# Performance work log

Measured on AMD Instinct MI355X. Metric: run time of the kernel, lower is better.

## Reference

```python
import jax, jax.numpy as jnp
import numpy as np

IN_F = 2048
OUT_F = 2048
BATCH = 16384
BASE_SPARSITY = 0.02
REVIVAL_DENSITY = 0.2   # rows for dead ('low') output neurons
RELIEF_DENSITY = 0.15   # cols for saturated ('high') input neurons
DEAD = np.arange(16)                      # 'low' extrema (row indices)
SATURATED = np.arange(100, 900, 100)      # 'high' extrema (col indices)


def _make_mask(key):
    k1, k2, k3 = jax.random.split(key, 3)
    base = (jax.random.uniform(k1, (OUT_F, IN_F)) < BASE_SPARSITY).astype(jnp.float32)
    patch = jnp.zeros((OUT_F, IN_F), jnp.float32)
    # dense-ish rows for dead output neurons
    row_patch = (jax.random.uniform(k2, (len(DEAD), IN_F)) < REVIVAL_DENSITY).astype(jnp.float32)
    patch = patch.at[jnp.asarray(DEAD), :].set(row_patch)
    # dense-ish cols for saturated input neurons (overwrite, matching torch order)
    col_patch = (jax.random.uniform(k3, (OUT_F, len(SATURATED))) < RELIEF_DENSITY).astype(jnp.float32)
    patch = patch.at[:, jnp.asarray(SATURATED)].set(col_patch)
    return jnp.maximum(base, patch)


def setup_inputs() -> dict:
    key = jax.random.key(0)
    kx, kw, km = jax.random.split(key, 3)
    x = jax.random.normal(kx, (BATCH, IN_F), dtype=jnp.float32)
    # kaiming_uniform_(a=sqrt(5)) -> U(-bound, bound), bound = sqrt(6/((1+a^2)*fan_in)) = 1/sqrt(fan_in)
    bound = 1.0 / np.sqrt(IN_F)
    weight = jax.random.uniform(kw, (OUT_F, IN_F), minval=-bound, maxval=bound, dtype=jnp.float32)
    bias = jnp.zeros((OUT_F,), jnp.float32)
    mask = _make_mask(km)
    return {"x": x, "weight": weight, "bias": bias, "mask": mask}


def reference(x, weight, bias, mask):
    # F.linear(x, weight * mask, bias): y = x @ (W*M)^T + b
    return jnp.einsum('bi,oi->bo', x, weight * mask) + bias
```

## Files before the change

### kernel.cpp

```cpp
#include <hip/hip_runtime.h>
#include <stdint.h>

#define BATCH 16384
#define IN_F 2048
#define OUT_F 2048

typedef unsigned short u16;
typedef __attribute__((ext_vector_type(8))) short bf16x8;
typedef __attribute__((ext_vector_type(4))) float f32x4;

__device__ __forceinline__ u16 f2bf(float f) {
  union { float f; uint32_t u; } v; v.f = f;
  uint32_t u = v.u;
  u += 0x7FFFu + ((u >> 16) & 1u);
  return (u16)(u >> 16);
}


__global__ void cvt_fused(const float4* __restrict__ x, const float4* __restrict__ w,
                          const float4* __restrict__ m, u16* __restrict__ xb,
                          u16* __restrict__ wb) {
  const int NX = BATCH * IN_F / 4;
  int i = blockIdx.x * 256 + threadIdx.x;
  if (i < NX) {
    float4 v = x[i];
    uint2 p;
    p.x = (uint32_t)f2bf(v.x) | ((uint32_t)f2bf(v.y) << 16);
    p.y = (uint32_t)f2bf(v.z) | ((uint32_t)f2bf(v.w) << 16);
    ((uint2*)xb)[i] = p;
  } else {
    int j = i - NX;
    float4 wv = w[j];
    float4 mv = m[j];
    uint2 p;
    p.x = (uint32_t)f2bf(wv.x * mv.x) | ((uint32_t)f2bf(wv.y * mv.y) << 16);
    p.y = (uint32_t)f2bf(wv.z * mv.z) | ((uint32_t)f2bf(wv.w * mv.w) << 16);
    ((uint2*)wb)[j] = p;
  }
}


__device__ __forceinline__ void async_cp16(const void* g, void* l) {
  __builtin_amdgcn_global_load_lds(
      (const __attribute__((address_space(1))) void*)g,
      (__attribute__((address_space(3))) void*)l,
      16, 0, 0);
}


#define BK 32
#define NT (IN_F / BK)

__global__ __launch_bounds__(512, 2) void gemm_bf16(const u16* __restrict__ A,
                                                    const u16* __restrict__ B,
                                                    const float* __restrict__ bias,
                                                    float* __restrict__ C) {
  __shared__ __align__(128) char smem[4 * 32768];
  const int K = IN_F, N = OUT_F;
  const int tid = threadIdx.x;
  const int lane = tid & 63, wave = tid >> 6;
  const int wm = wave >> 2;
  const int wn = wave & 3;
  const long bn = (long)blockIdx.x * 256;
  const long bm = (long)blockIdx.y * 256;

  const int sr = tid >> 2, sc = tid & 3;
  const int scs = sc ^ ((sr >> 1) & 3);
  const u16* gA = A + (bm + sr) * K + scs * 8;
  const u16* gB = B + (bn + sr) * K + scs * 8;
  const long hiK = 128L * K;
  const int ldst = tid * 16;

  auto stageA = [&](int slot, int kt) {
    char* sb = smem + slot * 32768;
    const long ko = (long)kt * BK;
    async_cp16(gA + ko, sb + ldst);
    async_cp16(gA + hiK + ko, sb + 8192 + ldst);
  };
  auto stageB = [&](int slot, int kt) {
    char* sb = smem + slot * 32768 + 16384;
    const long ko = (long)kt * BK;
    async_cp16(gB + ko, sb + ldst);
    async_cp16(gB + hiK + ko, sb + 8192 + ldst);
  };

  const int rl = lane & 15;
  const int q = lane >> 4;
  const int fb = rl * 64 + ((q ^ ((rl >> 1) & 3)) * 16);
  const int aoff = wm * 8192;
  const int boff = 16384 + wn * 4096;

  f32x4 acc[8][4];
#pragma unroll
  for (int i = 0; i < 8; i++)
#pragma unroll
    for (int j = 0; j < 4; j++)
#pragma unroll
      for (int r = 0; r < 4; r++) acc[i][j][r] = 0.0f;

  stageA(0, 0); stageB(0, 0);
  stageA(1, 1); stageB(1, 1);
  stageA(2, 2); stageB(2, 2);
  asm volatile("s_waitcnt vmcnt(4)" ::: "memory");
  __builtin_amdgcn_s_barrier();

  bf16x8 afA[4], bfA[4], afB[4], bfB[4];
#pragma unroll
  for (int i = 0; i < 4; i++) afA[i] = *(const bf16x8*)(smem + aoff + i * 1024 + fb);
#pragma unroll
  for (int j = 0; j < 4; j++) bfA[j] = *(const bf16x8*)(smem + boff + j * 1024 + fb);

#define BODY(T, curA, curB, nxtA, nxtB)                                          \
  do {                                                                           \
    const int t_ = (T);                                                          \
    const int slot_ = t_ & 3, s1_ = (t_ + 1) & 3, s3_ = (t_ + 3) & 3;            \
    const int kt3_ = (t_ + 3 < NT) ? t_ + 3 : NT - 1;                            \
    const char* sA_ = smem + slot_ * 32768 + aoff;                               \
    const char* sA1_ = smem + s1_ * 32768 + aoff;                                \
    const char* sB1_ = smem + s1_ * 32768 + boff;                                \
    stageA(s3_, kt3_);                                                           \
    stageB(s3_, kt3_);                                                           \
    bf16x8 af1_[4];                                                              \
    _Pragma("unroll")                                                            \
    for (int i = 0; i < 4; i++) af1_[i] = *(const bf16x8*)(sA_ + 4096 + i * 1024 + fb); \
    __builtin_amdgcn_s_setprio(1);                                               \
    _Pragma("unroll")                                                            \
    for (int i = 0; i < 4; i++)                                                  \
      _Pragma("unroll")                                                          \
      for (int j = 0; j < 4; j++)                                                \
        acc[i][j] = __builtin_amdgcn_mfma_f32_16x16x32_bf16(curA[i], curB[j], acc[i][j], 0, 0, 0); \
    __builtin_amdgcn_s_setprio(0);                                               \
    _Pragma("unroll")                                                            \
    for (int i = 0; i < 4; i++) nxtA[i] = *(const bf16x8*)(sA1_ + i * 1024 + fb); \
    _Pragma("unroll")                                                            \
    for (int j = 0; j < 4; j++) nxtB[j] = *(const bf16x8*)(sB1_ + j * 1024 + fb); \
    __builtin_amdgcn_s_setprio(1);                                               \
    _Pragma("unroll")                                                            \
    for (int i = 0; i < 4; i++)                                                  \
      _Pragma("unroll")                                                          \
      for (int j = 0; j < 4; j++)                                                \
        acc[4 + i][j] = __builtin_amdgcn_mfma_f32_16x16x32_bf16(af1_[i], curB[j], acc[4 + i][j], 0, 0, 0); \
    __builtin_amdgcn_s_setprio(0);                                               \
    asm volatile("s_waitcnt vmcnt(4)" ::: "memory");                             \
    __builtin_amdgcn_s_barrier();                                                \
  } while (0)

  for (int t = 0; t < NT; t += 2) {
    BODY(t, afA, bfA, afB, bfB);
    BODY(t + 1, afB, bfB, afA, bfA);
  }
#undef BODY

  asm volatile("s_waitcnt vmcnt(0)" ::: "memory");

  const int cn = lane & 15;
  const int crow = (lane >> 4) * 4;
#pragma unroll
  for (int j = 0; j < 4; j++) {
    const long n = bn + wn * 64 + j * 16 + cn;
    const float bv = bias[n];
#pragma unroll
    for (int i = 0; i < 8; i++) {
      const long m0 = bm + wm * 128 + i * 16 + crow;
      float* cp = C + m0 * N + n;
#pragma unroll
      for (int r = 0; r < 4; r++)
        cp[(long)r * N] = acc[i][j][r] + bv;
    }
  }
}


__global__ void naive_kernel(const float* __restrict__ x, const float* __restrict__ w,
                             const float* __restrict__ bias, const float* __restrict__ m,
                             float* __restrict__ out) {
  size_t idx = (size_t)blockIdx.x * 256 + threadIdx.x;
  int o = (int)(idx % OUT_F);
  size_t b = idx / OUT_F;
  float s = bias[o];
  const float* xr = x + b * IN_F;
  const float* wr = w + (size_t)o * IN_F;
  const float* mr = m + (size_t)o * IN_F;
  for (int k = 0; k < IN_F; k++) s += xr[k] * wr[k] * mr[k];
  out[idx] = s;
}

extern "C" void kernel_launch(void* const* d_in, const int* in_sizes, int n_in,
                              void* d_out, int out_size, void* d_ws, size_t ws_size,
                              hipStream_t stream) {
  const float* x = (const float*)d_in[0];
  const float* w = (const float*)d_in[1];
  const float* bias = (const float*)d_in[2];
  const float* mask = (const float*)d_in[3];
  float* out = (float*)d_out;

  const size_t xb_elems = (size_t)BATCH * IN_F;
  const size_t wm_elems = (size_t)OUT_F * IN_F;
  const size_t need = (xb_elems + wm_elems) * sizeof(u16);

  if (ws_size >= need) {
    u16* xb = (u16*)d_ws;
    u16* wm = xb + xb_elems;
    const uint32_t nblk = (uint32_t)((xb_elems + wm_elems) / 4 / 256);
    cvt_fused<<<nblk, 256, 0, stream>>>((const float4*)x, (const float4*)w,
                                        (const float4*)mask, xb, wm);
    gemm_bf16<<<dim3(OUT_F / 256, BATCH / 256), 512, 0, stream>>>(xb, wm, bias, out);
  } else {
    naive_kernel<<<(uint32_t)(((size_t)BATCH * OUT_F) / 256), 256, 0, stream>>>(x, w, bias, mask, out);
  }
}
```

Before: 360.6 us.

## Switch GEMM inner loop from 16x16x32 to 32x32x16 bf16 MFMA tiles

Replaces the 16x16x32 MFMA fragments with 32x32x16 bf16 MFMA, which changes the per-wave fragment layout, the LDS read addressing (with the same swizzle), the accumulator shape and the output store mapping. The loop is also unrolled by four so that LDS slot indices become compile-time constants. The larger MFMA is meant to cut the number of instructions and the LDS fragment reads per FLOP, but the epilogue now issues strided stores in a different pattern.

```diff
diff --git a/kernel.cpp b/kernel.cpp
--- a/kernel.cpp
+++ b/kernel.cpp
@@ -7,7 +7,7 @@
 
 typedef unsigned short u16;
 typedef __attribute__((ext_vector_type(8))) short bf16x8;
-typedef __attribute__((ext_vector_type(4))) float f32x4;
+typedef __attribute__((ext_vector_type(16))) float f32x16;
 
 __device__ __forceinline__ u16 f2bf(float f) {
   union { float f; uint32_t u; } v; v.f = f;
@@ -84,19 +84,26 @@
     async_cp16(gB + hiK + ko, sb + 8192 + ldst);
   };
 
-  const int rl = lane & 15;
-  const int q = lane >> 4;
-  const int fb = rl * 64 + ((q ^ ((rl >> 1) & 3)) * 16);
-  const int aoff = wm * 8192;
-  const int boff = 16384 + wn * 4096;
-
-  f32x4 acc[8][4];
-#pragma unroll
-  for (int i = 0; i < 8; i++)
-#pragma unroll
-    for (int j = 0; j < 4; j++)
-#pragma unroll
-      for (int r = 0; r < 4; r++) acc[i][j][r] = 0.0f;
+  const int r32 = lane & 31;
+  const int kq = lane >> 5;
+  const int xr = (r32 >> 1) & 3;
+  const int co0 = ((0 + kq) ^ xr) * 16;
+  const int co1 = ((2 + kq) ^ xr) * 16;
+  const int abase = wm * 8192 + r32 * 64;
+  const int bbase = 16384 + wn * 4096 + r32 * 64;
+
+#define LDA(SLOT, SUB, KS) \
+  (*(const bf16x8*)(smem + (SLOT) * 32768 + abase + (SUB) * 2048 + ((KS) ? co1 : co0)))
+#define LDB(SLOT, J, KS) \
+  (*(const bf16x8*)(smem + (SLOT) * 32768 + bbase + (J) * 2048 + ((KS) ? co1 : co0)))
+
+  f32x16 acc[4][2];
+#pragma unroll
+  for (int i = 0; i < 4; i++)
+#pragma unroll
+    for (int j = 0; j < 2; j++)
+#pragma unroll
+      for (int r = 0; r < 16; r++) acc[i][j][r] = 0.0f;
 
   stageA(0, 0); stageB(0, 0);
   stageA(1, 1); stageB(1, 1);
@@ -106,66 +113,82 @@
 
   bf16x8 afA[4], bfA[4], afB[4], bfB[4];
 #pragma unroll
-  for (int i = 0; i < 4; i++) afA[i] = *(const bf16x8*)(smem + aoff + i * 1024 + fb);
-#pragma unroll
-  for (int j = 0; j < 4; j++) bfA[j] = *(const bf16x8*)(smem + boff + j * 1024 + fb);
-
-#define BODY(T, curA, curB, nxtA, nxtB)                                          \
+  for (int i = 0; i < 2; i++) {
+    afA[i * 2 + 0] = LDA(0, i, 0);
+    afA[i * 2 + 1] = LDA(0, i, 1);
+    bfA[i * 2 + 0] = LDB(0, i, 0);
+    bfA[i * 2 + 1] = LDB(0, i, 1);
+  }
+
+#define BODY(T, SLOT, curA, curB, nxtA, nxtB)                                    \
   do {                                                                           \
     const int t_ = (T);                                                          \
-    const int slot_ = t_ & 3, s1_ = (t_ + 1) & 3, s3_ = (t_ + 3) & 3;            \
-    const int kt3_ = (t_ + 3 < NT) ? t_ + 3 : NT - 1;                            \
-    const char* sA_ = smem + slot_ * 32768 + aoff;                               \
-    const char* sA1_ = smem + s1_ * 32768 + aoff;                                \
-    const char* sB1_ = smem + s1_ * 32768 + boff;                                \
-    stageA(s3_, kt3_);                                                           \
-    stageB(s3_, kt3_);                                                           \
+    const int kt3_ = (t_ + 3 < NT) ? (t_ + 3) : (NT - 1);                        \
+    stageA(((SLOT) + 3) & 3, kt3_);                                              \
+    stageB(((SLOT) + 3) & 3, kt3_);                                              \
     bf16x8 af1_[4];                                                              \
     _Pragma("unroll")                                                            \
-    for (int i = 0; i < 4; i++) af1_[i] = *(const bf16x8*)(sA_ + 4096 + i * 1024 + fb); \
+    for (int i = 0; i < 2; i++) {                                                \
+      af1_[i * 2 + 0] = LDA(SLOT, 2 + i, 0);                                     \
+      af1_[i * 2 + 1] = LDA(SLOT, 2 + i, 1);                                     \
+    }                                                                            \
     __builtin_amdgcn_s_setprio(1);                                               \
     _Pragma("unroll")                                                            \
-    for (int i = 0; i < 4; i++)                                                  \
+    for (int ks = 0; ks < 2; ks++)                                               \
       _Pragma("unroll")                                                          \
-      for (int j = 0; j < 4; j++)                                                \
-        acc[i][j] = __builtin_amdgcn_mfma_f32_16x16x32_bf16(curA[i], curB[j], acc[i][j], 0, 0, 0); \
+      for (int i = 0; i < 2; i++)                                                \
+        _Pragma("unroll")                                                        \
+        for (int j = 0; j < 2; j++)                                              \
+          acc[i][j] = __builtin_amdgcn_mfma_f32_32x32x16_bf16(                   \
+              curA[i * 2 + ks], curB[j * 2 + ks], acc[i][j], 0, 0, 0);           \
     __builtin_amdgcn_s_setprio(0);                                               \
     _Pragma("unroll")                                                            \
-    for (int i = 0; i < 4; i++) nxtA[i] = *(const bf16x8*)(sA1_ + i * 1024 + fb); \
-    _Pragma("unroll")                                                            \
-    for (int j = 0; j < 4; j++) nxtB[j] = *(const bf16x8*)(sB1_ + j * 1024 + fb); \
+    for (int i = 0; i < 2; i++) {                                                \
+      nxtA[i * 2 + 0] = LDA(((SLOT) + 1) & 3, i, 0);                             \
+      nxtA[i * 2 + 1] = LDA(((SLOT) + 1) & 3, i, 1);                             \
+      nxtB[i * 2 + 0] = LDB(((SLOT) + 1) & 3, i, 0);                             \
+      nxtB[i * 2 + 1] = LDB(((SLOT) + 1) & 3, i, 1);                             \
+    }                                                                            \
     __builtin_amdgcn_s_setprio(1);                                               \
     _Pragma("unroll")                                                            \
-    for (int i = 0; i < 4; i++)                                                  \
+    for (int ks = 0; ks < 2; ks++)                                               \
       _Pragma("unroll")                                                          \
-      for (int j = 0; j < 4; j++)                                                \
-        acc[4 + i][j] = __builtin_amdgcn_mfma_f32_16x16x32_bf16(af1_[i], curB[j], acc[4 + i][j], 0, 0, 0); \
+      for (int i = 0; i < 2; i++)                                                \
+        _Pragma("unroll")                                                        \
+        for (int j = 0; j < 2; j++)                                              \
+          acc[2 + i][j] = __builtin_amdgcn_mfma_f32_32x32x16_bf16(               \
+              af1_[i * 2 + ks], curB[j * 2 + ks], acc[2 + i][j], 0, 0, 0);       \
     __builtin_amdgcn_s_setprio(0);                                               \
     asm volatile("s_waitcnt vmcnt(4)" ::: "memory");                             \
     __builtin_amdgcn_s_barrier();                                                \
   } while (0)
 
-  for (int t = 0; t < NT; t += 2) {
-    BODY(t, afA, bfA, afB, bfB);
-    BODY(t + 1, afB, bfB, afA, bfA);
+  for (int t = 0; t < NT; t += 4) {
+    BODY(t + 0, 0, afA, bfA, afB, bfB);
+    BODY(t + 1, 1, afB, bfB, afA, bfA);
+    BODY(t + 2, 2, afA, bfA, afB, bfB);
+    BODY(t + 3, 3, afB, bfB, afA, bfA);
   }
 #undef BODY
+#undef LDA
+#undef LDB
 
   asm volatile("s_waitcnt vmcnt(0)" ::: "memory");
 
-  const int cn = lane & 15;
-  const int crow = (lane >> 4) * 4;
-#pragma unroll
-  for (int j = 0; j < 4; j++) {
-    const long n = bn + wn * 64 + j * 16 + cn;
+  const int c32 = lane & 31;
+  const int rq4 = (lane >> 5) * 4;
+#pragma unroll
+  for (int j = 0; j < 2; j++) {
+    const long n = bn + wn * 64 + j * 32 + c32;
     const float bv = bias[n];
 #pragma unroll
-    for (int i = 0; i < 8; i++) {
-      const long m0 = bm + wm * 128 + i * 16 + crow;
-      float* cp = C + m0 * N + n;
-#pragma unroll
-      for (int r = 0; r < 4; r++)
-        cp[(long)r * N] = acc[i][j][r] + bv;
+    for (int i = 0; i < 4; i++) {
+      const long m0 = bm + wm * 128 + i * 32 + rq4;
+#pragma unroll
+      for (int reg = 0; reg < 16; reg++) {
+        const int row = (reg & 3) + 8 * (reg >> 2);
+        C[(m0 + row) * (long)N + n] = acc[i][j][reg] + bv;
+      }
     }
   }
 }
```

After: 365.8 us. No clear change (+1.4%).

## Load B fragments directly from global into registers, keep only A in LDS

Applied to the files above, without the earlier changes.

The weight (B) operand no longer goes through shared memory. Each wave loads its B fragments straight from global memory into registers one k-step ahead, and only A stays in the 4-slot LDS ring, which halves the LDS footprint. The main loop is unrolled by four so slot indices are compile-time constants, and the wait count is tightened to match. This removes the LDS writes and reads for B and may let two blocks share a CU, but each B global load's latency must now be hidden within a single iteration, and the two waves sharing a column tile fetch the same B data redundantly.

```diff
diff --git a/kernel.cpp b/kernel.cpp
--- a/kernel.cpp
+++ b/kernel.cpp
@@ -55,7 +55,7 @@
                                                     const u16* __restrict__ B,
                                                     const float* __restrict__ bias,
                                                     float* __restrict__ C) {
-  __shared__ __align__(128) char smem[4 * 32768];
+  __shared__ __align__(128) char smem[4 * 16384];
   const int K = IN_F, N = OUT_F;
   const int tid = threadIdx.x;
   const int lane = tid & 63, wave = tid >> 6;
@@ -67,28 +67,26 @@
   const int sr = tid >> 2, sc = tid & 3;
   const int scs = sc ^ ((sr >> 1) & 3);
   const u16* gA = A + (bm + sr) * K + scs * 8;
-  const u16* gB = B + (bn + sr) * K + scs * 8;
   const long hiK = 128L * K;
   const int ldst = tid * 16;
 
   auto stageA = [&](int slot, int kt) {
-    char* sb = smem + slot * 32768;
+    char* sb = smem + slot * 16384;
     const long ko = (long)kt * BK;
     async_cp16(gA + ko, sb + ldst);
     async_cp16(gA + hiK + ko, sb + 8192 + ldst);
   };
-  auto stageB = [&](int slot, int kt) {
-    char* sb = smem + slot * 32768 + 16384;
-    const long ko = (long)kt * BK;
-    async_cp16(gB + ko, sb + ldst);
-    async_cp16(gB + hiK + ko, sb + 8192 + ldst);
-  };
 
   const int rl = lane & 15;
   const int q = lane >> 4;
   const int fb = rl * 64 + ((q ^ ((rl >> 1) & 3)) * 16);
   const int aoff = wm * 8192;
-  const int boff = 16384 + wn * 4096;
+
+#define LDA(SLOT, I, HALF) \
+  (*(const bf16x8*)(smem + (SLOT) * 16384 + aoff + (HALF) * 4096 + (I) * 1024 + fb))
+
+  const u16* gBF = B + (bn + wn * 64 + rl) * (long)K + q * 8;
+#define LDBG(J, T) (*(const bf16x8*)(gBF + (long)(J) * (16 * 2048) + (T) * 32))
 
   f32x4 acc[8][4];
 #pragma unroll
@@ -98,58 +96,60 @@
 #pragma unroll
       for (int r = 0; r < 4; r++) acc[i][j][r] = 0.0f;
 
-  stageA(0, 0); stageB(0, 0);
-  stageA(1, 1); stageB(1, 1);
-  stageA(2, 2); stageB(2, 2);
-  asm volatile("s_waitcnt vmcnt(4)" ::: "memory");
+  bf16x8 afA[4], bfA[4], afB[4], bfB[4];
+#pragma unroll
+  for (int j = 0; j < 4; j++) bfA[j] = LDBG(j, 0);
+  stageA(0, 0);
+  stageA(1, 1);
+  stageA(2, 2);
+  asm volatile("s_waitcnt vmcnt(0)" ::: "memory");
   __builtin_amdgcn_s_barrier();
 
-  bf16x8 afA[4], bfA[4], afB[4], bfB[4];
-#pragma unroll
-  for (int i = 0; i < 4; i++) afA[i] = *(const bf16x8*)(smem + aoff + i * 1024 + fb);
-#pragma unroll
-  for (int j = 0; j < 4; j++) bfA[j] = *(const bf16x8*)(smem + boff + j * 1024 + fb);
-
-#define BODY(T, curA, curB, nxtA, nxtB)                                          \
+#pragma unroll
+  for (int i = 0; i < 4; i++) afA[i] = LDA(0, i, 0);
+
+#define BODY(T, SLOT, curAf, curB, nxtAf, nxtB)                                  \
   do {                                                                           \
     const int t_ = (T);                                                          \
-    const int slot_ = t_ & 3, s1_ = (t_ + 1) & 3, s3_ = (t_ + 3) & 3;            \
-    const int kt3_ = (t_ + 3 < NT) ? t_ + 3 : NT - 1;                            \
-    const char* sA_ = smem + slot_ * 32768 + aoff;                               \
-    const char* sA1_ = smem + s1_ * 32768 + aoff;                                \
-    const char* sB1_ = smem + s1_ * 32768 + boff;                                \
-    stageA(s3_, kt3_);                                                           \
-    stageB(s3_, kt3_);                                                           \
+    const int ktB_ = (t_ + 1 < NT) ? (t_ + 1) : (NT - 1);                        \
+    const int kt3_ = (t_ + 3 < NT) ? (t_ + 3) : (NT - 1);                        \
+    _Pragma("unroll")                                                            \
+    for (int j = 0; j < 4; j++) nxtB[j] = LDBG(j, ktB_);                         \
+    stageA(((SLOT) + 3) & 3, kt3_);                                              \
     bf16x8 af1_[4];                                                              \
     _Pragma("unroll")                                                            \
-    for (int i = 0; i < 4; i++) af1_[i] = *(const bf16x8*)(sA_ + 4096 + i * 1024 + fb); \
+    for (int i = 0; i < 4; i++) af1_[i] = LDA(SLOT, i, 1);                       \
     __builtin_amdgcn_s_setprio(1);                                               \
     _Pragma("unroll")                                                            \
     for (int i = 0; i < 4; i++)                                                  \
       _Pragma("unroll")                                                          \
       for (int j = 0; j < 4; j++)                                                \
-        acc[i][j] = __builtin_amdgcn_mfma_f32_16x16x32_bf16(curA[i], curB[j], acc[i][j], 0, 0, 0); \
+        acc[i][j] = __builtin_amdgcn_mfma_f32_16x16x32_bf16(                     \
+            curAf[i], curB[j], acc[i][j], 0, 0, 0);                              \
     __builtin_amdgcn_s_setprio(0);                                               \
     _Pragma("unroll")                                                            \
-    for (int i = 0; i < 4; i++) nxtA[i] = *(const bf16x8*)(sA1_ + i * 1024 + fb); \
-    _Pragma("unroll")                                                            \
-    for (int j = 0; j < 4; j++) nxtB[j] = *(const bf16x8*)(sB1_ + j * 1024 + fb); \
+    for (int i = 0; i < 4; i++) nxtAf[i] = LDA(((SLOT) + 1) & 3, i, 0);          \
     __builtin_amdgcn_s_setprio(1);                                               \
     _Pragma("unroll")                                                            \
     for (int i = 0; i < 4; i++)                                                  \
       _Pragma("unroll")                                                          \
       for (int j = 0; j < 4; j++)                                                \
-        acc[4 + i][j] = __builtin_amdgcn_mfma_f32_16x16x32_bf16(af1_[i], curB[j], acc[4 + i][j], 0, 0, 0); \
+        acc[4 + i][j] = __builtin_amdgcn_mfma_f32_16x16x32_bf16(                 \
+            af1_[i], curB[j], acc[4 + i][j], 0, 0, 0);                           \
     __builtin_amdgcn_s_setprio(0);                                               \
-    asm volatile("s_waitcnt vmcnt(4)" ::: "memory");                             \
+    asm volatile("s_waitcnt vmcnt(2)" ::: "memory");                             \
     __builtin_amdgcn_s_barrier();                                                \
   } while (0)
 
-  for (int t = 0; t < NT; t += 2) {
-    BODY(t, afA, bfA, afB, bfB);
-    BODY(t + 1, afB, bfB, afA, bfA);
+  for (int t = 0; t < NT; t += 4) {
+    BODY(t + 0, 0, afA, bfA, afB, bfB);
+    BODY(t + 1, 1, afB, bfB, afA, bfA);
+    BODY(t + 2, 2, afA, bfA, afB, bfB);
+    BODY(t + 3, 3, afB, bfB, afA, bfA);
   }
 #undef BODY
+#undef LDA
+#undef LDBG
 
   asm volatile("s_waitcnt vmcnt(0)" ::: "memory");
 
```

Result: slower. 443.2 us (+22.9%).
